# Kernel optimization log

Measured on AMD Instinct MI355X. Metric: run time of the kernel, lower is better.

## Reference

```python
import jax, jax.numpy as jnp
import numpy as np

D_MODEL = 1024
HEADS = 16
D_K = D_MODEL // HEADS
B, S = 2, 2048


def setup_inputs() -> dict:
    key = jax.random.key(0)
    ks = jax.random.split(key, 11)
    sc = 1.0 / np.sqrt(D_MODEL)
    inp = {
        "q": jax.random.normal(ks[0], (B, S, D_MODEL), jnp.float32),
        "k": jax.random.normal(ks[1], (B, S, D_MODEL), jnp.float32),
        "v": jax.random.normal(ks[2], (B, S, D_MODEL), jnp.float32),
        # causal mask, broadcastable to (B, H, S, S); 0 -> masked
        "mask": jnp.tril(jnp.ones((S, S), jnp.int32))[None, None],
        "w_q": jax.random.normal(ks[3], (D_MODEL, D_MODEL), jnp.float32) * sc,
        "b_q": jax.random.normal(ks[4], (D_MODEL,), jnp.float32) * sc,
        "w_k": jax.random.normal(ks[5], (D_MODEL, D_MODEL), jnp.float32) * sc,
        "b_k": jax.random.normal(ks[6], (D_MODEL,), jnp.float32) * sc,
        "w_v": jax.random.normal(ks[7], (D_MODEL, D_MODEL), jnp.float32) * sc,
        "b_v": jax.random.normal(ks[8], (D_MODEL,), jnp.float32) * sc,
        "w_o": jax.random.normal(ks[9], (D_MODEL, D_MODEL), jnp.float32) * sc,
        "b_o": jax.random.normal(ks[10], (D_MODEL,), jnp.float32) * sc,
    }
    return inp


def reference(q, k, v, mask, w_q, b_q, w_k, b_k, w_v, b_v, w_o, b_o):
    b = q.shape[0]
    # torch Linear: x @ W.T + b
    Q = q @ w_q.T + b_q
    K = k @ w_k.T + b_k
    V = v @ w_v.T + b_v
    # (B, S, D) -> (B, H, S, d_k)
    Q = Q.reshape(b, -1, HEADS, D_K).transpose(0, 2, 1, 3)
    K = K.reshape(b, -1, HEADS, D_K).transpose(0, 2, 1, 3)
    V = V.reshape(b, -1, HEADS, D_K).transpose(0, 2, 1, 3)
    scores = jnp.einsum("bhqd,bhkd->bhqk", Q, K) / np.sqrt(D_K).astype(np.float32)
    scores = jnp.where(mask == 0, -jnp.inf, scores)
    attn = jax.nn.softmax(scores, axis=-1)
    out = jnp.einsum("bhqk,bhkd->bhqd", attn, V)
    out = out.transpose(0, 2, 1, 3).reshape(b, -1, D_MODEL)
    # dropout is identity in eval mode
    return out @ w_o.T + b_o
```

## Files before the change

### kernel.cpp

```cpp
#include <hip/hip_runtime.h>
#include <math.h>

#define D_MODEL 1024
#define N_HEADS 16
#define DKH     64
#define BATCH   2
#define SEQ     2048
#define NT128   (SEQ/128)
#define PARTS_PER_BH 40

typedef unsigned short u16;
typedef unsigned long long u64;
typedef __attribute__((ext_vector_type(8))) short short8;
typedef __attribute__((ext_vector_type(4))) short s4v;
typedef __attribute__((ext_vector_type(4))) float f32x4;

__device__ __forceinline__ u16 f2bf(float f) {
    unsigned u = __float_as_uint(f);
    u += 0x7fffu + ((u >> 16) & 1u);
    return (u16)(u >> 16);
}
__device__ __forceinline__ float bf2f(u16 x) {
    return __int_as_float(((int)x) << 16);
}

__device__ __forceinline__ void gll16(const void* g, void* l) {
    __builtin_amdgcn_global_load_lds((const __attribute__((address_space(1))) void*)g,
                                     (__attribute__((address_space(3))) void*)l, 16, 0, 0);
}

__device__ __forceinline__ f32x4 mfma16(s4v a, s4v b, f32x4 c) {
#if __has_builtin(__builtin_amdgcn_mfma_f32_16x16x16bf16_1k)
    return __builtin_amdgcn_mfma_f32_16x16x16bf16_1k(a, b, c, 0, 0, 0);
#elif __has_builtin(__builtin_amdgcn_mfma_f32_16x16x16_bf16)
    return __builtin_amdgcn_mfma_f32_16x16x16_bf16(a, b, c, 0, 0, 0);
#else
    f32x4 d;
    asm("v_mfma_f32_16x16x16_bf16 %0, %1, %2, %3" : "=v"(d) : "v"(a), "v"(b), "v"(c));
    return d;
#endif
}

__global__ __launch_bounds__(256)
void convert_kernel(const float* __restrict__ q, const float* __restrict__ k,
                    const float* __restrict__ v, const float* __restrict__ wq,
                    const float* __restrict__ wk, const float* __restrict__ wv,
                    const float* __restrict__ wo,
                    u16* __restrict__ qb, u16* __restrict__ kb, u16* __restrict__ vb,
                    u16* __restrict__ wqb, u16* __restrict__ wkb,
                    u16* __restrict__ wvb, u16* __restrict__ wob)
{
    const size_t NV = ((size_t)16 << 20) >> 3;
    for (size_t i = (size_t)blockIdx.x * blockDim.x + threadIdx.x; i < NV;
         i += (size_t)gridDim.x * blockDim.x) {
        const size_t e = i << 3;
        const float* s; u16* d; size_t off;
        if (e < ((size_t)12 << 20)) {
            const int seg = (int)(e >> 22);
            off = e & (((size_t)1 << 22) - 1);
            s = seg == 0 ? q : seg == 1 ? k : v;
            d = seg == 0 ? qb : seg == 1 ? kb : vb;
        } else {
            const size_t r = e - ((size_t)12 << 20);
            const int seg = (int)(r >> 20);
            off = r & (((size_t)1 << 20) - 1);
            s = seg == 0 ? wq : seg == 1 ? wk : seg == 2 ? wv : wo;
            d = seg == 0 ? wqb : seg == 1 ? wkb : seg == 2 ? wvb : wob;
        }
        const float4 f0 = *(const float4*)(s + off);
        const float4 f1 = *(const float4*)(s + off + 4);
        short8 o;
        o[0]=(short)f2bf(f0.x); o[1]=(short)f2bf(f0.y); o[2]=(short)f2bf(f0.z); o[3]=(short)f2bf(f0.w);
        o[4]=(short)f2bf(f1.x); o[5]=(short)f2bf(f1.y); o[6]=(short)f2bf(f1.z); o[7]=(short)f2bf(f1.w);
        *(short8*)(d + off) = o;
    }
}

#define GEMM_PREAMBLE                                                            \
    __shared__ __align__(16) u16 As[2][128][32];                                 \
    __shared__ __align__(16) u16 Bs[2][128][32];                                 \
    const int tid  = threadIdx.x;                                                \
    const int lane = tid & 63;                                                   \
    const int wid  = tid >> 6;                                                   \
    const int wm   = wid >> 1, wn = wid & 1;                                     \
    const int lr   = lane & 15, lg = lane >> 4;                                  \
    const int mb   = blockIdx.x * 128, nb = blockIdx.y * 128;                    \
    const int g_row = lane >> 2;                                                 \
    const int g_col = (lane & 3) << 3;                                           \
    const u16* Ab = A  + (size_t)mb * K;                                         \
    const u16* Bb = Bw + (size_t)nb * K;                                         \
    f32x4 acc[4][4];                                                             \
    _Pragma("unroll")                                                            \
    for (int i = 0; i < 4; ++i)                                                  \
        _Pragma("unroll")                                                        \
        for (int j = 0; j < 4; ++j) { f32x4 z = {0.f,0.f,0.f,0.f}; acc[i][j] = z; }

#define STAGE(buf, kt)                                                           \
    {                                                                            \
        _Pragma("unroll")                                                        \
        for (int t = 0; t < 2; ++t) {                                            \
            const int r0 = t*64 + wid*16;                                        \
            gll16(&Ab[(size_t)(r0 + g_row)*K + (kt) + g_col], &As[buf][r0][0]);  \
            gll16(&Bb[(size_t)(r0 + g_row)*K + (kt) + g_col], &Bs[buf][r0][0]);  \
        }                                                                        \
    }

#define GEMM_MAINLOOP                                                            \
    STAGE(0, 0)                                                                  \
    __syncthreads();                                                             \
    const int NK = K >> 5;                                                       \
    for (int it = 0; it < NK; ++it) {                                            \
        const int c = it & 1;                                                    \
        if (it + 1 < NK) STAGE(c ^ 1, (it + 1) << 5)                             \
        short8 a[4], b[4];                                                       \
        _Pragma("unroll")                                                        \
        for (int i = 0; i < 4; ++i) a[i] = *(const short8*)&As[c][wm*64 + i*16 + lr][lg*8]; \
        _Pragma("unroll")                                                        \
        for (int j = 0; j < 4; ++j) b[j] = *(const short8*)&Bs[c][wn*64 + j*16 + lr][lg*8]; \
        _Pragma("unroll")                                                        \
        for (int i = 0; i < 4; ++i)                                              \
            _Pragma("unroll")                                                    \
            for (int j = 0; j < 4; ++j)                                          \
                acc[i][j] = __builtin_amdgcn_mfma_f32_16x16x32_bf16(a[i], b[j], acc[i][j], 0, 0, 0); \
        __syncthreads();                                                         \
    }

__global__ __launch_bounds__(256, 3)
void gemm_qkv_kernel(const u16* __restrict__ qb, const u16* __restrict__ kb,
                     const u16* __restrict__ vb, const u16* __restrict__ wqb,
                     const u16* __restrict__ wkb, const u16* __restrict__ wvb,
                     const float* __restrict__ b_q, const float* __restrict__ b_k,
                     const float* __restrict__ b_v,
                     u16* __restrict__ Qh, u16* __restrict__ Kh, u16* __restrict__ Vt,
                     int M, int N, int K)
{
    const int z = blockIdx.z;
    const u16* A    = z == 0 ? qb  : z == 1 ? kb  : vb;
    const u16* Bw   = z == 0 ? wqb : z == 1 ? wkb : wvb;
    const float* bias = z == 0 ? b_q : z == 1 ? b_k : b_v;
    u16* dst        = z == 0 ? Qh  : z == 1 ? Kh  : Vt;
    const float scale = z == 0 ? 0.125f : 1.0f;

    GEMM_PREAMBLE
    GEMM_MAINLOOP

    #pragma unroll
    for (int i = 0; i < 4; ++i) {
        #pragma unroll
        for (int j = 0; j < 4; ++j) {
            const int mbase = mb + wm*64 + i*16 + lg*4;
            const int n     = nb + wn*64 + j*16 + lr;
            const float bn  = bias[n];
            const int h = n >> 6, d = n & 63;
            #pragma unroll
            for (int r = 0; r < 4; ++r) {
                const int m = mbase + r;
                const int b = m >> 11, s = m & (SEQ - 1);
                const float val = (acc[i][j][r] + bn) * scale;
                if (z == 2)
                    dst[(((size_t)(b*N_HEADS + h))*DKH + d)*SEQ + s] = f2bf(val);
                else
                    dst[(((size_t)(b*N_HEADS + h))*SEQ + s)*DKH + d] = f2bf(val);
            }
        }
    }
}

__global__ __launch_bounds__(256)
void gemm_out_kernel(const u16* __restrict__ A, const u16* __restrict__ Bw,
                     const float* __restrict__ bias, float* __restrict__ dst,
                     int M, int N, int K)
{
    __shared__ __align__(16) u16 As[2][128][32];
    __shared__ __align__(16) u16 Bs[2][64][32];

    const int tid  = threadIdx.x;
    const int lane = tid & 63;
    const int wid  = tid >> 6;
    const int wm   = wid >> 1, wn = wid & 1;
    const int lr   = lane & 15, lg = lane >> 4;
    const int mb   = blockIdx.x * 128, nb = blockIdx.y * 64;
    const int g_row = lane >> 2;
    const int g_col = (lane & 3) << 3;

    const u16* Ab = A  + (size_t)mb * K;
    const u16* Bb = Bw + (size_t)nb * K;

    f32x4 acc[4][2];
    #pragma unroll
    for (int i = 0; i < 4; ++i)
        #pragma unroll
        for (int j = 0; j < 2; ++j) { f32x4 z = {0.f,0.f,0.f,0.f}; acc[i][j] = z; }

#define OSTAGE(buf, kt)                                                          \
    {                                                                            \
        _Pragma("unroll")                                                        \
        for (int t = 0; t < 2; ++t) {                                            \
            const int r0 = t*64 + wid*16;                                        \
            gll16(&Ab[(size_t)(r0 + g_row)*K + (kt) + g_col], &As[buf][r0][0]);  \
        }                                                                        \
        gll16(&Bb[(size_t)(wid*16 + g_row)*K + (kt) + g_col], &Bs[buf][wid*16][0]); \
    }

    OSTAGE(0, 0)
    __syncthreads();

    const int NK = K >> 5;
    for (int it = 0; it < NK; ++it) {
        const int c = it & 1;
        if (it + 1 < NK) OSTAGE(c ^ 1, (it + 1) << 5)

        short8 a[4], b[2];
        #pragma unroll
        for (int i = 0; i < 4; ++i) a[i] = *(const short8*)&As[c][wm*64 + i*16 + lr][lg*8];
        #pragma unroll
        for (int j = 0; j < 2; ++j) b[j] = *(const short8*)&Bs[c][wn*32 + j*16 + lr][lg*8];
        #pragma unroll
        for (int i = 0; i < 4; ++i)
            #pragma unroll
            for (int j = 0; j < 2; ++j)
                acc[i][j] = __builtin_amdgcn_mfma_f32_16x16x32_bf16(a[i], b[j], acc[i][j], 0, 0, 0);

        __syncthreads();
    }
#undef OSTAGE

    #pragma unroll
    for (int i = 0; i < 4; ++i) {
        #pragma unroll
        for (int j = 0; j < 2; ++j) {
            const int mbase = mb + wm*64 + i*16 + lg*4;
            const int n     = nb + wn*32 + j*16 + lr;
            const float bn  = bias[n];
            #pragma unroll
            for (int r = 0; r < 4; ++r)
                dst[(size_t)(mbase + r) * N + n] = acc[i][j][r] + bn;
        }
    }
}

__device__ __forceinline__ void attn_step(
    const short8& aq0, const short8& aq1,
    f32x4 (&o)[4], float& osum, float& m_run,
    const u16 (*__restrict__ Kl)[64], const u16 (*__restrict__ Vl)[64],
    int kvb, int qbw, int lr, int lg)
{
    const int ksw = (lr & 7) << 3;
    f32x4 st[4];
    __builtin_amdgcn_s_setprio(1);
    #pragma unroll
    for (int c = 0; c < 4; ++c) {
        const int kr = c*16 + lr;
        f32x4 z = {0.f,0.f,0.f,0.f};
        short8 k0 = *(const short8*)&Kl[kr][( 0 + lg*8) ^ ksw];
        short8 k1 = *(const short8*)&Kl[kr][(32 + lg*8) ^ ksw];
        z = __builtin_amdgcn_mfma_f32_16x16x32_bf16(k0, aq0, z, 0, 0, 0);
        z = __builtin_amdgcn_mfma_f32_16x16x32_bf16(k1, aq1, z, 0, 0, 0);
        st[c] = z;
    }
    __builtin_amdgcn_s_setprio(0);

    if (kvb + 63 > qbw) {
        #pragma unroll
        for (int c = 0; c < 4; ++c)
            #pragma unroll
            for (int r = 0; r < 4; ++r)
                if (kvb + c*16 + lg*4 + r > qbw + lr) st[c][r] = -INFINITY;
    }

    float tm = fmaxf(fmaxf(st[0][0], st[0][1]), fmaxf(st[0][2], st[0][3]));
    #pragma unroll
    for (int c = 1; c < 4; ++c)
        tm = fmaxf(tm, fmaxf(fmaxf(st[c][0], st[c][1]), fmaxf(st[c][2], st[c][3])));
    tm = fmaxf(tm, __shfl_xor(tm, 16));
    tm = fmaxf(tm, __shfl_xor(tm, 32));

    if (__any(tm > m_run + 8.f)) {
        const float mnew  = fmaxf(m_run, tm);
        const float alpha = __expf(m_run - mnew);
        m_run = mnew;
        osum *= alpha;
        float af[4];
        #pragma unroll
        for (int r = 0; r < 4; ++r)
            af[r] = __shfl(alpha, (lg << 4) | (lg*4 + r));
        #pragma unroll
        for (int db = 0; db < 4; ++db)
            #pragma unroll
            for (int r = 0; r < 4; ++r) o[db][r] *= af[r];
    }

    s4v av[4];
    float sum = 0.f;
    #pragma unroll
    for (int c = 0; c < 4; ++c) {
        const float p0 = __expf(st[c][0] - m_run);
        const float p1 = __expf(st[c][1] - m_run);
        const float p2 = __expf(st[c][2] - m_run);
        const float p3 = __expf(st[c][3] - m_run);
        sum += (p0 + p1) + (p2 + p3);
        unsigned lo, hi;
        asm("v_cvt_pk_bf16_f32 %0, %1, %2" : "=v"(lo) : "v"(p0), "v"(p1));
        asm("v_cvt_pk_bf16_f32 %0, %1, %2" : "=v"(hi) : "v"(p2), "v"(p3));
        union { unsigned u[2]; s4v s; } uu;
        uu.u[0] = lo; uu.u[1] = hi;
        av[c] = uu.s;
    }
    osum += sum;

    __builtin_amdgcn_s_setprio(1);
    #pragma unroll
    for (int c = 0; c < 4; ++c) {
        #pragma unroll
        for (int db = 0; db < 4; ++db) {
            union { u64 q; s4v s; } bv;
            bv.q = *(const u64*)&Vl[db*16 + lr][(c*16 + lg*4) ^ ksw];
            o[db] = mfma16(av[c], bv.s, o[db]);
        }
    }
    __builtin_amdgcn_s_setprio(0);
}

__global__ __launch_bounds__(512)
void flash_split_kernel(const u16* __restrict__ Qh, const u16* __restrict__ Kh,
                        const u16* __restrict__ Vt, u16* __restrict__ part_o,
                        float* __restrict__ part_ms)
{
    __shared__ __align__(16) u16 Kl[64][64];
    __shared__ __align__(16) u16 Vl[64][64];

    const int x = blockIdx.x;
    int t, ch;
    if      (x <  4) { t = x;                 ch = 0;        }
    else if (x < 12) { t = 4 + ((x-4) >> 1);  ch = (x-4)&1;  }
    else if (x < 24) { t = 8 + (x-12)/3;      ch = (x-12)%3; }
    else             { t = 12 + ((x-24) >> 2); ch = (x-24)&3; }

    const int tid  = threadIdx.x;
    const int lane = tid & 63;
    const int wid  = tid >> 6;
    const int lr   = lane & 15, lg = lane >> 4;
    const int bh   = blockIdx.y;
    const int qbw  = t*128 + wid*16;
    const size_t base = (size_t)bh * SEQ * DKH;

    const int c0      = ch * 8;
    const int nc_here = min(8, 2*(t+1) - c0);

    const int srow = tid >> 3;
    const int se0  = (tid & 7) << 3;
    const int sec  = se0 ^ ((srow & 7) << 3);

    short8 aq0 = *(const short8*)&Qh[base + (size_t)(qbw + lr)*DKH +  0 + lg*8];
    short8 aq1 = *(const short8*)&Qh[base + (size_t)(qbw + lr)*DKH + 32 + lg*8];

    f32x4 o[4];
    float osum = 0.f, m_run = -INFINITY;
    {
        f32x4 z = {0.f,0.f,0.f,0.f};
        #pragma unroll
        for (int db = 0; db < 4; ++db) o[db] = z;
    }

    {
        const int kb0 = c0 * 64;
        short8 k0 = *(const short8*)&Kh[base + (size_t)(kb0 + srow)*DKH + se0];
        short8 v0 = *(const short8*)&Vt[base + (size_t)srow*SEQ + kb0 + se0];
        *(short8*)&Kl[srow][sec] = k0;
        *(short8*)&Vl[srow][sec] = v0;
    }
    __syncthreads();

    for (int ci = 0; ci < nc_here; ++ci) {
        const int kvb = (c0 + ci) * 64;
        short8 nk0, nv0;
        const bool pref = (ci + 1 < nc_here);
        if (pref) {
            const int nb_ = kvb + 64;
            nk0 = *(const short8*)&Kh[base + (size_t)(nb_ + srow)*DKH + se0];
            nv0 = *(const short8*)&Vt[base + (size_t)srow*SEQ + nb_ + se0];
        }

        if (kvb <= qbw + 15)
            attn_step(aq0, aq1, o, osum, m_run, Kl, Vl, kvb, qbw, lr, lg);

        __syncthreads();
        if (pref) {
            *(short8*)&Kl[srow][sec] = nk0;
            *(short8*)&Vl[srow][sec] = nv0;
        }
        __syncthreads();
    }

    osum += __shfl_xor(osum, 16);
    osum += __shfl_xor(osum, 32);

    const size_t slot = (size_t)bh * PARTS_PER_BH + x;
    u16*   po = part_o  + (slot << 13);
    float* pm = part_ms + (slot << 8);
    #pragma unroll
    for (int db = 0; db < 4; ++db)
        #pragma unroll
        for (int r = 0; r < 4; ++r)
            po[(wid*16 + lg*4 + r)*64 + db*16 + lr] = f2bf(o[db][r]);
    if (lane < 16) {
        pm[(wid*16 + lane)*2 + 0] = m_run;
        pm[(wid*16 + lane)*2 + 1] = osum;
    }
}

__global__ __launch_bounds__(256)
void merge_kernel(const u16* __restrict__ part_o, const float* __restrict__ part_ms,
                  u16* __restrict__ attb)
{
    const int t   = blockIdx.x;
    const int bh  = blockIdx.y;
    const int nch = min(4, (2*(t+1) + 7) >> 3);
    const int basex = t < 4 ? t : t < 8 ? 4 + 2*(t-4) : t < 12 ? 12 + 3*(t-8) : 24 + 4*(t-12);

    const int row = threadIdx.x >> 1;
    const int cb  = (threadIdx.x & 1) * 32;

    float mm[4], ss[4];
    float M = -INFINITY;
    for (int c = 0; c < nch; ++c) {
        const size_t slot = (size_t)bh * PARTS_PER_BH + basex + c;
        mm[c] = part_ms[(slot << 8) + row*2 + 0];
        ss[c] = part_ms[(slot << 8) + row*2 + 1];
        M = fmaxf(M, mm[c]);
    }
    float S = 0.f;
    float acc[32];
    #pragma unroll
    for (int j = 0; j < 32; ++j) acc[j] = 0.f;
    for (int c = 0; c < nch; ++c) {
        const float w = __expf(mm[c] - M);
        S += w * ss[c];
        const size_t slot = (size_t)bh * PARTS_PER_BH + basex + c;
        const u16* po = part_o + (slot << 13) + row*64 + cb;
        #pragma unroll
        for (int g = 0; g < 4; ++g) {
            short8 v = *(const short8*)(po + g*8);
            #pragma unroll
            for (int j = 0; j < 8; ++j)
                acc[g*8 + j] += w * bf2f((u16)v[j]);
        }
    }
    const float inv = 1.f / S;
    const int b = bh >> 4, h = bh & 15;
    const int grow = t*128 + row;
    u16* dst = attb + ((size_t)(b*SEQ + grow))*D_MODEL + h*64 + cb;
    #pragma unroll
    for (int g = 0; g < 4; ++g) {
        short8 ov;
        #pragma unroll
        for (int j = 0; j < 8; ++j) ov[j] = (short)f2bf(acc[g*8 + j] * inv);
        *(short8*)(dst + g*8) = ov;
    }
}

extern "C" void kernel_launch(void* const* d_in, const int* in_sizes, int n_in,
                              void* d_out, int out_size, void* d_ws, size_t ws_size,
                              hipStream_t stream)
{
    const float* q   = (const float*)d_in[0];
    const float* k   = (const float*)d_in[1];
    const float* v   = (const float*)d_in[2];
    const float* w_q = (const float*)d_in[4];
    const float* b_q = (const float*)d_in[5];
    const float* w_k = (const float*)d_in[6];
    const float* b_k = (const float*)d_in[7];
    const float* w_v = (const float*)d_in[8];
    const float* b_v = (const float*)d_in[9];
    const float* w_o = (const float*)d_in[10];
    const float* b_o = (const float*)d_in[11];

    char* ws = (char*)d_ws;
    const size_t MB = 1024*1024;
    u16* Qh   = (u16*)(ws +  0*MB);
    u16* Kh   = (u16*)(ws +  8*MB);
    u16* Vt   = (u16*)(ws + 16*MB);
    u16* qb   = (u16*)(ws + 24*MB);
    u16* kb   = (u16*)(ws + 32*MB);
    u16* vb   = (u16*)(ws + 40*MB);
    u16* wqb  = (u16*)(ws + 48*MB);
    u16* wkb  = (u16*)(ws + 50*MB);
    u16* wvb  = (u16*)(ws + 52*MB);
    u16* wob  = (u16*)(ws + 54*MB);
    u16* attb = qb;
    u16*   part_o  = (u16*)(ws + 32*MB);
    float* part_ms = (float*)(ws + 52*MB);

    const int M = BATCH * SEQ, N = D_MODEL, K = D_MODEL;

    convert_kernel<<<2048, 256, 0, stream>>>(q, k, v, w_q, w_k, w_v, w_o,
                                             qb, kb, vb, wqb, wkb, wvb, wob);
    gemm_qkv_kernel<<<dim3(M/128, N/128, 3), 256, 0, stream>>>(
        qb, kb, vb, wqb, wkb, wvb, b_q, b_k, b_v, Qh, Kh, Vt, M, N, K);
    flash_split_kernel<<<dim3(PARTS_PER_BH, BATCH*N_HEADS), 512, 0, stream>>>(
        Qh, Kh, Vt, part_o, part_ms);
    merge_kernel<<<dim3(NT128, BATCH*N_HEADS), 256, 0, stream>>>(part_o, part_ms, attb);
    gemm_out_kernel<<<dim3(M/128, N/64), 256, 0, stream>>>(attb, wob, b_o, (float*)d_out, M, N, K);
}
```

Before: 136.7 us.

## Double-buffer K/V tiles via direct global-to-LDS loads and reverse block order

```diff
diff --git a/kernel.cpp b/kernel.cpp
--- a/kernel.cpp
+++ b/kernel.cpp
@@ -326,10 +326,10 @@
                         const u16* __restrict__ Vt, u16* __restrict__ part_o,
                         float* __restrict__ part_ms)
 {
-    __shared__ __align__(16) u16 Kl[64][64];
-    __shared__ __align__(16) u16 Vl[64][64];
-
-    const int x = blockIdx.x;
+    __shared__ __align__(16) u16 Kl[2][64][64];
+    __shared__ __align__(16) u16 Vl[2][64][64];
+
+    const int x = 39 - blockIdx.x;
     int t, ch;
     if      (x <  4) { t = x;                 ch = 0;        }
     else if (x < 12) { t = 4 + ((x-4) >> 1);  ch = (x-4)&1;  }
@@ -347,9 +347,15 @@
     const int c0      = ch * 8;
     const int nc_here = min(8, 2*(t+1) - c0);
 
-    const int srow = tid >> 3;
-    const int se0  = (tid & 7) << 3;
-    const int sec  = se0 ^ ((srow & 7) << 3);
+    const int srow8 = lane >> 3;
+    const int srow  = wid*8 + srow8;
+    const int scol  = ((lane & 7) << 3) ^ (srow8 << 3);
+
+#define FSTAGE(buf, kb)                                                          \
+    {                                                                            \
+        gll16(&Kh[base + (size_t)((kb) + srow)*DKH + scol], &Kl[buf][wid*8][0]); \
+        gll16(&Vt[base + (size_t)srow*SEQ + (kb) + scol],  &Vl[buf][wid*8][0]);  \
+    }
 
     short8 aq0 = *(const short8*)&Qh[base + (size_t)(qbw + lr)*DKH +  0 + lg*8];
     short8 aq1 = *(const short8*)&Qh[base + (size_t)(qbw + lr)*DKH + 32 + lg*8];
@@ -362,35 +368,20 @@
         for (int db = 0; db < 4; ++db) o[db] = z;
     }
 
-    {
-        const int kb0 = c0 * 64;
-        short8 k0 = *(const short8*)&Kh[base + (size_t)(kb0 + srow)*DKH + se0];
-        short8 v0 = *(const short8*)&Vt[base + (size_t)srow*SEQ + kb0 + se0];
-        *(short8*)&Kl[srow][sec] = k0;
-        *(short8*)&Vl[srow][sec] = v0;
-    }
+    FSTAGE(0, c0*64)
     __syncthreads();
 
     for (int ci = 0; ci < nc_here; ++ci) {
+        const int p = ci & 1;
+        if (ci + 1 < nc_here) FSTAGE(p ^ 1, (c0 + ci + 1)*64)
+
         const int kvb = (c0 + ci) * 64;
-        short8 nk0, nv0;
-        const bool pref = (ci + 1 < nc_here);
-        if (pref) {
-            const int nb_ = kvb + 64;
-            nk0 = *(const short8*)&Kh[base + (size_t)(nb_ + srow)*DKH + se0];
-            nv0 = *(const short8*)&Vt[base + (size_t)srow*SEQ + nb_ + se0];
-        }
-
         if (kvb <= qbw + 15)
-            attn_step(aq0, aq1, o, osum, m_run, Kl, Vl, kvb, qbw, lr, lg);
+            attn_step(aq0, aq1, o, osum, m_run, Kl[p], Vl[p], kvb, qbw, lr, lg);
 
         __syncthreads();
-        if (pref) {
-            *(short8*)&Kl[srow][sec] = nk0;
-            *(short8*)&Vl[srow][sec] = nv0;
-        }
-        __syncthreads();
-    }
+    }
+#undef FSTAGE
 
     osum += __shfl_xor(osum, 16);
     osum += __shfl_xor(osum, 32);
```

After: 135.8 us. About the same (-0.7%).
